# Performance work log

Hardware: AMD Instinct MI355X
Metric: run time of the kernel (lower is better)

## Reference

```python
import jax, jax.numpy as jnp
import numpy as np
import math

EMB_DIM = 1024
HEADS = 16
HEAD_DIM = EMB_DIM // HEADS
B, S = 2, 2048


def setup_inputs() -> dict:
    key = jax.random.key(0)
    k1, k2, k3, k4, k5 = jax.random.split(key, 5)
    X = jax.random.normal(k1, (B, S, EMB_DIM), dtype=jnp.float32)
    # causal mask: positions with 0.0 are masked to -inf (masked_fill(mask == 0.0, -inf))
    mask = jnp.tril(jnp.ones((S, S), dtype=jnp.float32))
    scale = 1.0 / math.sqrt(EMB_DIM)
    # torch Linear(emb_dim, 3*emb_dim): y = x @ W.T + b; store W pre-transposed [E, 3E]
    W_qkv = jax.random.normal(k2, (EMB_DIM, 3 * EMB_DIM), dtype=jnp.float32) * scale
    b_qkv = jnp.zeros((3 * EMB_DIM,), dtype=jnp.float32)
    W_o = jax.random.normal(k3, (EMB_DIM, EMB_DIM), dtype=jnp.float32) * scale
    b_o = jnp.zeros((EMB_DIM,), dtype=jnp.float32)
    return {"X": X, "mask": mask, "W_qkv": W_qkv, "b_qkv": b_qkv, "W_o": W_o, "b_o": b_o}


def reference(X, mask, W_qkv, b_qkv, W_o, b_o):
    # X: [B, S, E]
    Bn, Sn, E = X.shape
    qkv = X @ W_qkv + b_qkv                                   # [B, S, 3E]
    qkv = qkv.reshape(Bn, Sn, 3, HEADS, HEAD_DIM)
    qkv = jnp.transpose(qkv, (2, 0, 3, 1, 4))                  # [3, B, H, S, d]
    Q, K, V = qkv[0], qkv[1], qkv[2]
    inv_sqrt_d = 1.0 / math.sqrt(HEAD_DIM)
    scores = jnp.einsum('bhqd,bhkd->bhqk', Q, K) * inv_sqrt_d  # [B, H, S, S]
    scores = jnp.where(mask == 0.0, -jnp.inf, scores)
    attn = jax.nn.softmax(scores, axis=-1)
    # dropout omitted (eval mode / deterministic reference)
    out = jnp.einsum('bhqk,bhkd->bhqd', attn, V)               # [B, H, S, d]
    out = jnp.transpose(out, (0, 2, 1, 3)).reshape(Bn, Sn, E)
    return out @ W_o + b_o
```

## Files before the change

### kernel.cpp

```cpp
#include <hip/hip_runtime.h>
#include <hip/hip_bf16.h>
#include <cstdint>
#include <cstddef>

typedef __bf16 bf16_t;
typedef __attribute__((ext_vector_type(8))) __bf16 bf16x8;
typedef __attribute__((ext_vector_type(4))) __bf16 bf16x4;
typedef __attribute__((ext_vector_type(4))) float f32x4;

#define AS1 __attribute__((address_space(1)))
#define AS3 __attribute__((address_space(3)))

static constexpr int Bn = 2, Sn = 2048, En = 1024, Hn = 16, Dn = 64;

__global__ __launch_bounds__(256) void convert_f32_bf16(
    const float* __restrict__ in, bf16_t* __restrict__ out, int n) {
  int i = (blockIdx.x * 256 + threadIdx.x) * 4;
  if (i < n) {
    float4 v = *(const float4*)(in + i);
    bf16x4 o;
    o[0] = (bf16_t)v.x; o[1] = (bf16_t)v.y; o[2] = (bf16_t)v.z; o[3] = (bf16_t)v.w;
    *(bf16x4*)(out + i) = o;
  }
}

__global__ __launch_bounds__(256) void transpose_conv(
    const float* __restrict__ in, bf16_t* __restrict__ out, int R, int C) {
  __shared__ float tile[32][33];
  int bx = blockIdx.x * 32, by = blockIdx.y * 32;
  int tx = threadIdx.x & 31, ty = threadIdx.x >> 5;
#pragma unroll
  for (int i = 0; i < 32; i += 8)
    tile[ty + i][tx] = in[(size_t)(by + ty + i) * C + bx + tx];
  __syncthreads();
#pragma unroll
  for (int i = 0; i < 32; i += 8)
    out[(size_t)(bx + ty + i) * R + by + tx] = (bf16_t)tile[tx][ty + i];
}

__global__ __launch_bounds__(256) void transpose_v(
    const bf16_t* __restrict__ V, bf16_t* __restrict__ Vt) {
  __shared__ ushort tile[64][65];
  int bh = blockIdx.y, s0 = blockIdx.x * 64;
  int t = threadIdx.x;
  const ushort* src = (const ushort*)(V + ((size_t)bh * Sn + s0) * 64);
#pragma unroll
  for (int p = 0; p < 4; ++p) {
    int s = p * 16 + (t >> 4);
    int c = (t & 15) * 4;
    ushort4 v = *(const ushort4*)(src + (size_t)s * 64 + c);
    tile[s][c] = v.x; tile[s][c + 1] = v.y; tile[s][c + 2] = v.z; tile[s][c + 3] = v.w;
  }
  __syncthreads();
  ushort* dst = (ushort*)(Vt + ((size_t)bh * 64) * Sn + s0);
#pragma unroll
  for (int p = 0; p < 4; ++p) {
    int d = p * 16 + (t >> 4);
    int c = (t & 15) * 4;
    ushort4 v;
    v.x = tile[c][d]; v.y = tile[c + 1][d]; v.z = tile[c + 2][d]; v.w = tile[c + 3][d];
    *(ushort4*)(dst + (size_t)d * Sn + c) = v;
  }
}

template <int K_>
__device__ __forceinline__ void gemm_core(
    const bf16_t* __restrict__ A, const bf16_t* __restrict__ Bt,
    f32x4 (&acc)[4][4], int& col0, int& row0) {
  __shared__ bf16_t As[2][128 * 32];
  __shared__ bf16_t Bs[2][128 * 32];
  const int tid = threadIdx.x, lane = tid & 63, wid = tid >> 6;
  const int wm = wid >> 1, wn = wid & 1;
  const int m0 = blockIdx.y * 128, n0 = blockIdx.x * 128;
  const int KT = K_ / 32;

  auto stage = [&](bf16_t* as, bf16_t* bs, int kt) {
    int csw = ((lane & 3) ^ ((lane >> 2) & 3)) * 8;
#pragma unroll
    for (int j = 0; j < 2; ++j) {
      int r0 = wid * 32 + j * 16;
      const bf16_t* ga = A + (size_t)(m0 + r0 + (lane >> 2)) * K_ + kt * 32 + csw;
      __builtin_amdgcn_global_load_lds((const AS1 void*)ga, (AS3 void*)(as + r0 * 32), 16, 0, 0);
      const bf16_t* gb = Bt + (size_t)(n0 + r0 + (lane >> 2)) * K_ + kt * 32 + csw;
      __builtin_amdgcn_global_load_lds((const AS1 void*)gb, (AS3 void*)(bs + r0 * 32), 16, 0, 0);
    }
  };
  auto compute = [&](const bf16_t* as, const bf16_t* bs) {
    bf16x8 af[4], bfr[4];
    uint32_t swz = (uint32_t)(((lane >> 4) ^ (lane & 3)) << 4);
#pragma unroll
    for (int mi = 0; mi < 4; ++mi) {
      uint32_t row = (uint32_t)(wm * 64 + mi * 16 + (lane & 15));
      af[mi] = *(const bf16x8*)((const char*)as + row * 64 + swz);
    }
#pragma unroll
    for (int ni = 0; ni < 4; ++ni) {
      uint32_t row = (uint32_t)(wn * 64 + ni * 16 + (lane & 15));
      bfr[ni] = *(const bf16x8*)((const char*)bs + row * 64 + swz);
    }
#pragma unroll
    for (int mi = 0; mi < 4; ++mi)
#pragma unroll
      for (int ni = 0; ni < 4; ++ni)
        acc[mi][ni] = __builtin_amdgcn_mfma_f32_16x16x32_bf16(af[mi], bfr[ni], acc[mi][ni], 0, 0, 0);
  };

  stage(As[0], Bs[0], 0);
  __syncthreads();
  int cur = 0;
  for (int kt = 0; kt < KT - 1; ++kt) {
    stage(As[cur ^ 1], Bs[cur ^ 1], kt + 1);
    compute(As[cur], Bs[cur]);
    __syncthreads();
    cur ^= 1;
  }
  compute(As[cur], Bs[cur]);
  col0 = n0 + wn * 64 + (lane & 15);
  row0 = m0 + wm * 64 + ((lane >> 4) << 2);
}

__global__ __launch_bounds__(256) void gemm_qkv(
    const bf16_t* __restrict__ A, const bf16_t* __restrict__ Bt,
    const float* __restrict__ bias, bf16_t* __restrict__ Qb,
    bf16_t* __restrict__ Kb, bf16_t* __restrict__ Vb) {
  f32x4 acc[4][4] = {};
  int col0, row0;
  gemm_core<1024>(A, Bt, acc, col0, row0);
#pragma unroll
  for (int ni = 0; ni < 4; ++ni) {
    int n = col0 + ni * 16;
    float bv = bias[n];
    int which = n >> 10, nn = n & 1023;
    int h = nn >> 6, dd = nn & 63;
    bf16_t* dst = which == 0 ? Qb : (which == 1 ? Kb : Vb);
    float scl = which == 0 ? 0.125f : 1.0f;
#pragma unroll
    for (int mi = 0; mi < 4; ++mi)
#pragma unroll
      for (int i = 0; i < 4; ++i) {
        int m = row0 + mi * 16 + i;
        int b = m >> 11, s = m & 2047;
        float v = (acc[mi][ni][i] + bv) * scl;
        dst[(((size_t)b * Hn + h) * Sn + s) * 64 + dd] = (bf16_t)v;
      }
  }
}

__global__ __launch_bounds__(256) void gemm_out(
    const bf16_t* __restrict__ A, const bf16_t* __restrict__ Bt,
    const float* __restrict__ bias, float* __restrict__ out) {
  f32x4 acc[4][4] = {};
  int col0, row0;
  gemm_core<1024>(A, Bt, acc, col0, row0);
#pragma unroll
  for (int ni = 0; ni < 4; ++ni) {
    int n = col0 + ni * 16;
    float bv = bias[n];
#pragma unroll
    for (int mi = 0; mi < 4; ++mi)
#pragma unroll
      for (int i = 0; i < 4; ++i) {
        int m = row0 + mi * 16 + i;
        out[(size_t)m * En + n] = acc[mi][ni][i] + bv;
      }
  }
}

__global__ __launch_bounds__(256) void attn_fwd(
    const bf16_t* __restrict__ Qb, const bf16_t* __restrict__ Kb,
    const bf16_t* __restrict__ Vt, bf16_t* __restrict__ AO) {
  __shared__ bf16_t Ks[2][64 * 64];
  __shared__ bf16_t Vs[2][64 * 64];
  __shared__ bf16_t Ps[4][16 * 64];
  const int tid = threadIdx.x, lane = tid & 63, wid = tid >> 6;
  const int bh = blockIdx.y;
  const int q_tile = (int)(blockIdx.x ^ blockIdx.y) & 31;
  const int q0 = q_tile * 64;
  const int qb = q0 + wid * 16;

  bf16x8 aq[2];
  {
    const bf16_t* qp = Qb + ((size_t)bh * Sn + qb + (lane & 15)) * 64 + ((lane >> 4) << 3);
    aq[0] = *(const bf16x8*)qp;
    aq[1] = *(const bf16x8*)(qp + 32);
  }
  f32x4 O[4] = {};
  float m_run[4], l_run[4];
#pragma unroll
  for (int i = 0; i < 4; ++i) { m_run[i] = -1e30f; l_run[i] = 0.f; }

  const int rl = lane >> 3;
  const int cp = lane & 7;
  auto issueKV = [&](int buf, int t) {
#pragma unroll
    for (int j = 0; j < 2; ++j) {
      int r = wid * 16 + j * 8 + rl;
      int sc = cp ^ (r & 7);
      const bf16_t* gk = Kb + (((size_t)bh * Sn + t * 64 + r) << 6) + (sc << 3);
      __builtin_amdgcn_global_load_lds((const AS1 void*)gk,
          (AS3 void*)(&Ks[buf][wid * 1024 + j * 512]), 16, 0, 0);
      const bf16_t* gv = Vt + ((size_t)bh * 64 + r) * Sn + t * 64 + (sc << 3);
      __builtin_amdgcn_global_load_lds((const AS1 void*)gv,
          (AS3 void*)(&Vs[buf][wid * 1024 + j * 512]), 16, 0, 0);
    }
  };

  const int nt = q_tile + 1;
  issueKV(0, 0);
  for (int t = 0; t < nt; ++t) {
    const int cur = t & 1;
    asm volatile("s_waitcnt vmcnt(0)" ::: "memory");
    __syncthreads();
    if (t + 1 < nt) issueKV(cur ^ 1, t + 1);
    const char* ksb = (const char*)Ks[cur];
    const char* vsb = (const char*)Vs[cur];
    f32x4 sc[4];
#pragma unroll
    for (int ni = 0; ni < 4; ++ni) {
      int kvr = ni * 16 + (lane & 15);
      uint32_t o0 = (uint32_t)(kvr * 128 + ((lane >> 4) << 4)) ^ (uint32_t)((kvr & 7) << 4);
      uint32_t o1 = (uint32_t)(kvr * 128 + 64 + ((lane >> 4) << 4)) ^ (uint32_t)((kvr & 7) << 4);
      bf16x8 b0 = *(const bf16x8*)(ksb + o0);
      bf16x8 b1 = *(const bf16x8*)(ksb + o1);
      f32x4 z = {};
      z = __builtin_amdgcn_mfma_f32_16x16x32_bf16(aq[0], b0, z, 0, 0, 0);
      sc[ni] = __builtin_amdgcn_mfma_f32_16x16x32_bf16(aq[1], b1, z, 0, 0, 0);
    }
    if (t == nt - 1) {
#pragma unroll
      for (int ni = 0; ni < 4; ++ni) {
        int kv = t * 64 + ni * 16 + (lane & 15);
#pragma unroll
        for (int i = 0; i < 4; ++i) {
          int q = qb + ((lane >> 4) << 2) + i;
          if (kv > q) sc[ni][i] = -1e30f;
        }
      }
    }
    float mt[4];
#pragma unroll
    for (int i = 0; i < 4; ++i) {
      float v = fmaxf(fmaxf(sc[0][i], sc[1][i]), fmaxf(sc[2][i], sc[3][i]));
      v = fmaxf(v, __shfl_xor(v, 1));
      v = fmaxf(v, __shfl_xor(v, 2));
      v = fmaxf(v, __shfl_xor(v, 4));
      v = fmaxf(v, __shfl_xor(v, 8));
      mt[i] = v;
    }
    float scale[4], rs[4];
#pragma unroll
    for (int i = 0; i < 4; ++i) {
      float mn = fmaxf(m_run[i], mt[i]);
      scale[i] = __expf(m_run[i] - mn);
      m_run[i] = mn;
      rs[i] = 0.f;
    }
    char* pw = (char*)Ps[wid];
#pragma unroll
    for (int ni = 0; ni < 4; ++ni)
#pragma unroll
      for (int i = 0; i < 4; ++i) {
        float p = __expf(sc[ni][i] - m_run[i]);
        rs[i] += p;
        int r = ((lane >> 4) << 2) + i;
        uint32_t off = (uint32_t)(r * 128 + (ni * 16 + (lane & 15)) * 2) ^ (uint32_t)((r & 7) << 4);
        *(bf16_t*)(pw + off) = (bf16_t)p;
      }
#pragma unroll
    for (int i = 0; i < 4; ++i) {
      float v = rs[i];
      v += __shfl_xor(v, 1);
      v += __shfl_xor(v, 2);
      v += __shfl_xor(v, 4);
      v += __shfl_xor(v, 8);
      l_run[i] = l_run[i] * scale[i] + v;
    }
#pragma unroll
    for (int n2 = 0; n2 < 4; ++n2)
#pragma unroll
      for (int i = 0; i < 4; ++i) O[n2][i] *= scale[i];
    asm volatile("s_waitcnt lgkmcnt(0)" ::: "memory");
    __builtin_amdgcn_sched_barrier(0);
    bf16x8 pa[2];
    {
      int r = lane & 15;
      uint32_t o0 = (uint32_t)(r * 128 + ((lane >> 4) << 4)) ^ (uint32_t)((r & 7) << 4);
      uint32_t o1 = (uint32_t)(r * 128 + 64 + ((lane >> 4) << 4)) ^ (uint32_t)((r & 7) << 4);
      pa[0] = *(const bf16x8*)((const char*)pw + o0);
      pa[1] = *(const bf16x8*)((const char*)pw + o1);
    }
#pragma unroll
    for (int n2 = 0; n2 < 4; ++n2) {
      int dr = n2 * 16 + (lane & 15);
      uint32_t o0 = (uint32_t)(dr * 128 + ((lane >> 4) << 4)) ^ (uint32_t)((dr & 7) << 4);
      uint32_t o1 = (uint32_t)(dr * 128 + 64 + ((lane >> 4) << 4)) ^ (uint32_t)((dr & 7) << 4);
      bf16x8 v0 = *(const bf16x8*)(vsb + o0);
      bf16x8 v1 = *(const bf16x8*)(vsb + o1);
      O[n2] = __builtin_amdgcn_mfma_f32_16x16x32_bf16(pa[0], v0, O[n2], 0, 0, 0);
      O[n2] = __builtin_amdgcn_mfma_f32_16x16x32_bf16(pa[1], v1, O[n2], 0, 0, 0);
    }
  }
  int b = bh >> 4, h = bh & 15;
#pragma unroll
  for (int i = 0; i < 4; ++i) {
    float inv = 1.0f / l_run[i];
    int q = qb + ((lane >> 4) << 2) + i;
#pragma unroll
    for (int n2 = 0; n2 < 4; ++n2) {
      int d = n2 * 16 + (lane & 15);
      AO[((size_t)b * Sn + q) * En + h * 64 + d] = (bf16_t)(O[n2][i] * inv);
    }
  }
}

extern "C" void kernel_launch(void* const* d_in, const int* in_sizes, int n_in,
                              void* d_out, int out_size, void* d_ws, size_t ws_size,
                              hipStream_t stream) {
  const float* X     = (const float*)d_in[0];
  const float* W_qkv = (const float*)d_in[2];
  const float* b_qkv = (const float*)d_in[3];
  const float* W_o   = (const float*)d_in[4];
  const float* b_o   = (const float*)d_in[5];
  float* out = (float*)d_out;

  char* ws = (char*)d_ws;
  bf16_t* Xb  = (bf16_t*)(ws);
  bf16_t* WqT = (bf16_t*)(ws + 8388608);
  bf16_t* WoT = (bf16_t*)(ws + 14680064);
  bf16_t* Qb  = (bf16_t*)(ws + 16777216);
  bf16_t* Kb  = (bf16_t*)(ws + 25165824);
  bf16_t* Vb  = (bf16_t*)(ws + 33554432);
  bf16_t* Vt  = (bf16_t*)(ws + 41943040);
  bf16_t* AO  = (bf16_t*)(ws + 50331648);

  convert_f32_bf16<<<4096, 256, 0, stream>>>(X, Xb, Bn * Sn * En);
  transpose_conv<<<dim3(96, 32), 256, 0, stream>>>(W_qkv, WqT, 1024, 3072);
  transpose_conv<<<dim3(32, 32), 256, 0, stream>>>(W_o, WoT, 1024, 1024);
  gemm_qkv<<<dim3(24, 32), 256, 0, stream>>>(Xb, WqT, b_qkv, Qb, Kb, Vb);
  transpose_v<<<dim3(32, 32), 256, 0, stream>>>(Vb, Vt);
  attn_fwd<<<dim3(32, 32), 256, 0, stream>>>(Qb, Kb, Vt, AO);
  gemm_out<<<dim3(8, 32), 256, 0, stream>>>(AO, WoT, b_o, out);
}
```

Baseline: 265.3 us.

## Pair causal query tiles per block and add lazy softmax rescaling

Each attention block now handles two query tiles, pr and 31-pr, so every block does the same total number of KV iterations under the causal mask. The grid is halved to 512 blocks, and the first KV tile of the second segment is prefetched while the first segment finishes. It also adds a wave-uniform lazy rescale: the running max and the O/l accumulators are only updated when some row's tile max exceeds the old max by more than 8. That removes most exp and multiply work per tile, at the cost of larger unnormalised partial sums and fewer blocks to fill the GPU's compute units.

```diff
diff --git a/kernel.cpp b/kernel.cpp
--- a/kernel.cpp
+++ b/kernel.cpp
@@ -174,20 +174,7 @@
   __shared__ bf16_t Ps[4][16 * 64];
   const int tid = threadIdx.x, lane = tid & 63, wid = tid >> 6;
   const int bh = blockIdx.y;
-  const int q_tile = (int)(blockIdx.x ^ blockIdx.y) & 31;
-  const int q0 = q_tile * 64;
-  const int qb = q0 + wid * 16;
-
-  bf16x8 aq[2];
-  {
-    const bf16_t* qp = Qb + ((size_t)bh * Sn + qb + (lane & 15)) * 64 + ((lane >> 4) << 3);
-    aq[0] = *(const bf16x8*)qp;
-    aq[1] = *(const bf16x8*)(qp + 32);
-  }
-  f32x4 O[4] = {};
-  float m_run[4], l_run[4];
-#pragma unroll
-  for (int i = 0; i < 4; ++i) { m_run[i] = -1e30f; l_run[i] = 0.f; }
+  const int pr = blockIdx.x;
 
   const int rl = lane >> 3;
   const int cp = lane & 7;
@@ -205,110 +192,131 @@
     }
   };
 
-  const int nt = q_tile + 1;
+  int buf = 0;
   issueKV(0, 0);
-  for (int t = 0; t < nt; ++t) {
-    const int cur = t & 1;
-    asm volatile("s_waitcnt vmcnt(0)" ::: "memory");
-    __syncthreads();
-    if (t + 1 < nt) issueKV(cur ^ 1, t + 1);
-    const char* ksb = (const char*)Ks[cur];
-    const char* vsb = (const char*)Vs[cur];
-    f32x4 sc[4];
-#pragma unroll
-    for (int ni = 0; ni < 4; ++ni) {
-      int kvr = ni * 16 + (lane & 15);
-      uint32_t o0 = (uint32_t)(kvr * 128 + ((lane >> 4) << 4)) ^ (uint32_t)((kvr & 7) << 4);
-      uint32_t o1 = (uint32_t)(kvr * 128 + 64 + ((lane >> 4) << 4)) ^ (uint32_t)((kvr & 7) << 4);
-      bf16x8 b0 = *(const bf16x8*)(ksb + o0);
-      bf16x8 b1 = *(const bf16x8*)(ksb + o1);
-      f32x4 z = {};
-      z = __builtin_amdgcn_mfma_f32_16x16x32_bf16(aq[0], b0, z, 0, 0, 0);
-      sc[ni] = __builtin_amdgcn_mfma_f32_16x16x32_bf16(aq[1], b1, z, 0, 0, 0);
-    }
-    if (t == nt - 1) {
+
+  for (int seg = 0; seg < 2; ++seg) {
+    const int q_tile = seg ? 31 - pr : pr;
+    const int nt = q_tile + 1;
+    const int qb = q_tile * 64 + wid * 16;
+
+    bf16x8 aq[2];
+    {
+      const bf16_t* qp = Qb + ((size_t)bh * Sn + qb + (lane & 15)) * 64 + ((lane >> 4) << 3);
+      aq[0] = *(const bf16x8*)qp;
+      aq[1] = *(const bf16x8*)(qp + 32);
+    }
+    f32x4 O[4] = {};
+    float m_run[4], l_run[4];
+#pragma unroll
+    for (int i = 0; i < 4; ++i) { m_run[i] = -1e30f; l_run[i] = 0.f; }
+
+    for (int t = 0; t < nt; ++t) {
+      asm volatile("s_waitcnt vmcnt(0)" ::: "memory");
+      __syncthreads();
+      if (t + 1 < nt) issueKV(buf ^ 1, t + 1);
+      else if (seg == 0) issueKV(buf ^ 1, 0);
+      const char* ksb = (const char*)Ks[buf];
+      const char* vsb = (const char*)Vs[buf];
+      f32x4 sc[4];
 #pragma unroll
       for (int ni = 0; ni < 4; ++ni) {
-        int kv = t * 64 + ni * 16 + (lane & 15);
+        int kvr = ni * 16 + (lane & 15);
+        uint32_t o0 = (uint32_t)(kvr * 128 + ((lane >> 4) << 4)) ^ (uint32_t)((kvr & 7) << 4);
+        uint32_t o1 = (uint32_t)(kvr * 128 + 64 + ((lane >> 4) << 4)) ^ (uint32_t)((kvr & 7) << 4);
+        bf16x8 b0 = *(const bf16x8*)(ksb + o0);
+        bf16x8 b1 = *(const bf16x8*)(ksb + o1);
+        f32x4 z = {};
+        z = __builtin_amdgcn_mfma_f32_16x16x32_bf16(aq[0], b0, z, 0, 0, 0);
+        sc[ni] = __builtin_amdgcn_mfma_f32_16x16x32_bf16(aq[1], b1, z, 0, 0, 0);
+      }
+      if (t == nt - 1) {
+#pragma unroll
+        for (int ni = 0; ni < 4; ++ni) {
+          int kv = t * 64 + ni * 16 + (lane & 15);
+#pragma unroll
+          for (int i = 0; i < 4; ++i) {
+            int q = qb + ((lane >> 4) << 2) + i;
+            if (kv > q) sc[ni][i] = -1e30f;
+          }
+        }
+      }
+      float mt[4];
+#pragma unroll
+      for (int i = 0; i < 4; ++i) {
+        float v = fmaxf(fmaxf(sc[0][i], sc[1][i]), fmaxf(sc[2][i], sc[3][i]));
+        v = fmaxf(v, __shfl_xor(v, 1));
+        v = fmaxf(v, __shfl_xor(v, 2));
+        v = fmaxf(v, __shfl_xor(v, 4));
+        v = fmaxf(v, __shfl_xor(v, 8));
+        mt[i] = v;
+      }
+      int ok = (mt[0] <= m_run[0] + 8.f) && (mt[1] <= m_run[1] + 8.f) &&
+               (mt[2] <= m_run[2] + 8.f) && (mt[3] <= m_run[3] + 8.f);
+      if (!__all(ok)) {
 #pragma unroll
         for (int i = 0; i < 4; ++i) {
-          int q = qb + ((lane >> 4) << 2) + i;
-          if (kv > q) sc[ni][i] = -1e30f;
+          float mn = fmaxf(m_run[i], mt[i]);
+          float s = __expf(m_run[i] - mn);
+          m_run[i] = mn;
+          l_run[i] *= s;
+#pragma unroll
+          for (int n2 = 0; n2 < 4; ++n2) O[n2][i] *= s;
         }
       }
-    }
-    float mt[4];
+      float rs[4] = {0.f, 0.f, 0.f, 0.f};
+      char* pw = (char*)Ps[wid];
+#pragma unroll
+      for (int ni = 0; ni < 4; ++ni)
+#pragma unroll
+        for (int i = 0; i < 4; ++i) {
+          float p = __expf(sc[ni][i] - m_run[i]);
+          rs[i] += p;
+          int r = ((lane >> 4) << 2) + i;
+          uint32_t off = (uint32_t)(r * 128 + (ni * 16 + (lane & 15)) * 2) ^ (uint32_t)((r & 7) << 4);
+          *(bf16_t*)(pw + off) = (bf16_t)p;
+        }
+#pragma unroll
+      for (int i = 0; i < 4; ++i) {
+        float v = rs[i];
+        v += __shfl_xor(v, 1);
+        v += __shfl_xor(v, 2);
+        v += __shfl_xor(v, 4);
+        v += __shfl_xor(v, 8);
+        l_run[i] += v;
+      }
+      asm volatile("s_waitcnt lgkmcnt(0)" ::: "memory");
+      __builtin_amdgcn_sched_barrier(0);
+      bf16x8 pa[2];
+      {
+        int r = lane & 15;
+        uint32_t o0 = (uint32_t)(r * 128 + ((lane >> 4) << 4)) ^ (uint32_t)((r & 7) << 4);
+        uint32_t o1 = (uint32_t)(r * 128 + 64 + ((lane >> 4) << 4)) ^ (uint32_t)((r & 7) << 4);
+        pa[0] = *(const bf16x8*)((const char*)pw + o0);
+        pa[1] = *(const bf16x8*)((const char*)pw + o1);
+      }
+#pragma unroll
+      for (int n2 = 0; n2 < 4; ++n2) {
+        int dr = n2 * 16 + (lane & 15);
+        uint32_t o0 = (uint32_t)(dr * 128 + ((lane >> 4) << 4)) ^ (uint32_t)((dr & 7) << 4);
+        uint32_t o1 = (uint32_t)(dr * 128 + 64 + ((lane >> 4) << 4)) ^ (uint32_t)((dr & 7) << 4);
+        bf16x8 v0 = *(const bf16x8*)(vsb + o0);
+        bf16x8 v1 = *(const bf16x8*)(vsb + o1);
+        O[n2] = __builtin_amdgcn_mfma_f32_16x16x32_bf16(pa[0], v0, O[n2], 0, 0, 0);
+        O[n2] = __builtin_amdgcn_mfma_f32_16x16x32_bf16(pa[1], v1, O[n2], 0, 0, 0);
+      }
+      buf ^= 1;
+    }
+    int b = bh >> 4, h = bh & 15;
 #pragma unroll
     for (int i = 0; i < 4; ++i) {
-      float v = fmaxf(fmaxf(sc[0][i], sc[1][i]), fmaxf(sc[2][i], sc[3][i]));
-      v = fmaxf(v, __shfl_xor(v, 1));
-      v = fmaxf(v, __shfl_xor(v, 2));
-      v = fmaxf(v, __shfl_xor(v, 4));
-      v = fmaxf(v, __shfl_xor(v, 8));
-      mt[i] = v;
-    }
-    float scale[4], rs[4];
-#pragma unroll
-    for (int i = 0; i < 4; ++i) {
-      float mn = fmaxf(m_run[i], mt[i]);
-      scale[i] = __expf(m_run[i] - mn);
-      m_run[i] = mn;
-      rs[i] = 0.f;
-    }
-    char* pw = (char*)Ps[wid];
-#pragma unroll
-    for (int ni = 0; ni < 4; ++ni)
-#pragma unroll
-      for (int i = 0; i < 4; ++i) {
-        float p = __expf(sc[ni][i] - m_run[i]);
-        rs[i] += p;
-        int r = ((lane >> 4) << 2) + i;
-        uint32_t off = (uint32_t)(r * 128 + (ni * 16 + (lane & 15)) * 2) ^ (uint32_t)((r & 7) << 4);
-        *(bf16_t*)(pw + off) = (bf16_t)p;
-      }
-#pragma unroll
-    for (int i = 0; i < 4; ++i) {
-      float v = rs[i];
-      v += __shfl_xor(v, 1);
-      v += __shfl_xor(v, 2);
-      v += __shfl_xor(v, 4);
-      v += __shfl_xor(v, 8);
-      l_run[i] = l_run[i] * scale[i] + v;
-    }
-#pragma unroll
-    for (int n2 = 0; n2 < 4; ++n2)
-#pragma unroll
-      for (int i = 0; i < 4; ++i) O[n2][i] *= scale[i];
-    asm volatile("s_waitcnt lgkmcnt(0)" ::: "memory");
-    __builtin_amdgcn_sched_barrier(0);
-    bf16x8 pa[2];
-    {
-      int r = lane & 15;
-      uint32_t o0 = (uint32_t)(r * 128 + ((lane >> 4) << 4)) ^ (uint32_t)((r & 7) << 4);
-      uint32_t o1 = (uint32_t)(r * 128 + 64 + ((lane >> 4) << 4)) ^ (uint32_t)((r & 7) << 4);
-      pa[0] = *(const bf16x8*)((const char*)pw + o0);
-      pa[1] = *(const bf16x8*)((const char*)pw + o1);
-    }
-#pragma unroll
-    for (int n2 = 0; n2 < 4; ++n2) {
-      int dr = n2 * 16 + (lane & 15);
-      uint32_t o0 = (uint32_t)(dr * 128 + ((lane >> 4) << 4)) ^ (uint32_t)((dr & 7) << 4);
-      uint32_t o1 = (uint32_t)(dr * 128 + 64 + ((lane >> 4) << 4)) ^ (uint32_t)((dr & 7) << 4);
-      bf16x8 v0 = *(const bf16x8*)(vsb + o0);
-      bf16x8 v1 = *(const bf16x8*)(vsb + o1);
-      O[n2] = __builtin_amdgcn_mfma_f32_16x16x32_bf16(pa[0], v0, O[n2], 0, 0, 0);
-      O[n2] = __builtin_amdgcn_mfma_f32_16x16x32_bf16(pa[1], v1, O[n2], 0, 0, 0);
-    }
-  }
-  int b = bh >> 4, h = bh & 15;
-#pragma unroll
-  for (int i = 0; i < 4; ++i) {
-    float inv = 1.0f / l_run[i];
-    int q = qb + ((lane >> 4) << 2) + i;
-#pragma unroll
-    for (int n2 = 0; n2 < 4; ++n2) {
-      int d = n2 * 16 + (lane & 15);
-      AO[((size_t)b * Sn + q) * En + h * 64 + d] = (bf16_t)(O[n2][i] * inv);
+      float inv = 1.0f / l_run[i];
+      int q = qb + ((lane >> 4) << 2) + i;
+#pragma unroll
+      for (int n2 = 0; n2 < 4; ++n2) {
+        int d = n2 * 16 + (lane & 15);
+        AO[((size_t)b * Sn + q) * En + h * 64 + d] = (bf16_t)(O[n2][i] * inv);
+      }
     }
   }
 }
@@ -338,6 +346,6 @@
   transpose_conv<<<dim3(32, 32), 256, 0, stream>>>(W_o, WoT, 1024, 1024);
   gemm_qkv<<<dim3(24, 32), 256, 0, stream>>>(Xb, WqT, b_qkv, Qb, Kb, Vb);
   transpose_v<<<dim3(32, 32), 256, 0, stream>>>(Vb, Vt);
-  attn_fwd<<<dim3(32, 32), 256, 0, stream>>>(Qb, Kb, Vt, AO);
+  attn_fwd<<<dim3(16, 32), 256, 0, stream>>>(Qb, Kb, Vt, AO);
   gemm_out<<<dim3(8, 32), 256, 0, stream>>>(AO, WoT, b_o, out);
 }
```

Measured after the change: 239.3 us. -9.8%, faster.
